# Performance work log

Measured on AMD Instinct MI355X. Metric: run time of the kernel, lower is better.

Reference implementation:

```python
import jax, jax.numpy as jnp
import numpy as np

def setup_inputs() -> dict:
    key = jax.random.key(0)
    k1, k2 = jax.random.split(key)
    B, C = 65536, 1000
    outputs = jax.random.normal(k1, (B, C), dtype=jnp.float32)
    labels = jax.random.randint(k2, (B,), 0, C, dtype=jnp.int64)
    return {"outputs": outputs, "labels": labels}

def reference(outputs, labels):
    B = outputs.shape[0]
    # ground-truth score per row: [B, 1]
    ground = jnp.take_along_axis(outputs, labels[:, None].astype(jnp.int32), axis=1)
    # hinge margin per class: max(0, y_j - y_true + 1); j == label contributes exactly 1
    margins = jnp.maximum(outputs - ground + 1.0, 0.0)
    per_row = jnp.sum(margins, axis=1) - 1.0  # remove the j == label term
    loss = jnp.sum(per_row) / B
    correct_count = jnp.sum(jnp.argmax(outputs, axis=1) == labels)
    return (loss, correct_count)
```

## Files before the change

### kernel.cpp

```cpp
#include <hip/hip_runtime.h>
#include <hip/hip_bf16.h>
#include <math.h>


#define BLOCK 256
#define GRID 1024

__global__ __launch_bounds__(BLOCK) void msrp_kernel(
    const float* __restrict__ outp, const int* __restrict__ labels,
    float* __restrict__ dst, int B, int C) {
  const int lane = threadIdx.x & 63;
  const int wave_in_block = threadIdx.x >> 6;
  const int wave_id = (blockIdx.x * blockDim.x + threadIdx.x) >> 6;
  const int n_waves = (gridDim.x * blockDim.x) >> 6;
  const int C4 = C >> 2;

  float loss_acc = 0.0f;
  int correct_acc = 0;

  for (int row = wave_id; row < B; row += n_waves) {
    const float* rowp = outp + (size_t)row * (size_t)C;
    const int label = labels[row];
    const float ground = rowp[label];
    const float base = 1.0f - ground;

    const float4* rp4 = (const float4*)rowp;
    float s = 0.0f;
    float mx = -INFINITY;
    int mi = 0x7fffffff;

    for (int j = lane; j < C4; j += 64) {
      float4 v = rp4[j];
      s += fmaxf(v.x + base, 0.0f) + fmaxf(v.y + base, 0.0f) +
           fmaxf(v.z + base, 0.0f) + fmaxf(v.w + base, 0.0f);
      const int j4 = j << 2;
      if (v.x > mx) { mx = v.x; mi = j4; }
      if (v.y > mx) { mx = v.y; mi = j4 + 1; }
      if (v.z > mx) { mx = v.z; mi = j4 + 2; }
      if (v.w > mx) { mx = v.w; mi = j4 + 3; }
    }
    for (int j = (C4 << 2) + lane; j < C; j += 64) {
      float v = rowp[j];
      s += fmaxf(v + base, 0.0f);
      if (v > mx) { mx = v; mi = j; }
    }

    for (int off = 32; off > 0; off >>= 1) {
      s += __shfl_down(s, off, 64);
      float omx = __shfl_down(mx, off, 64);
      int omi = __shfl_down(mi, off, 64);
      if (omx > mx || (omx == mx && omi < mi)) { mx = omx; mi = omi; }
    }

    if (lane == 0) {
      loss_acc += s - 1.0f;
      correct_acc += (mi == label) ? 1 : 0;
    }
  }

  __shared__ float ls[BLOCK / 64];
  __shared__ int cs[BLOCK / 64];
  if (lane == 0) { ls[wave_in_block] = loss_acc; cs[wave_in_block] = correct_acc; }
  __syncthreads();
  if (threadIdx.x == 0) {
    float L = 0.0f;
    int cc = 0;
    for (int w = 0; w < BLOCK / 64; ++w) { L += ls[w]; cc += cs[w]; }
    atomicAdd(&dst[0], L / (float)B);
    atomicAdd(&dst[1], (float)cc);
  }
}

extern "C" void kernel_launch(void* const* d_in, const int* in_sizes, int n_in,
                              void* d_out, int out_size, void* d_ws, size_t ws_size,
                              hipStream_t stream) {
  const float* outp = (const float*)d_in[0];
  const int* labels = (const int*)d_in[1];
  float* dst = (float*)d_out;

  const int B = in_sizes[1];
  const int C = in_sizes[0] / B;

  hipMemsetAsync(d_out, 0, (size_t)out_size * sizeof(float), stream);

  msrp_kernel<<<GRID, BLOCK, 0, stream>>>(outp, labels, dst, B, C);
}
```

Measured before the change: 370.4 us.

## Replace argmax with ground-violation ballot and defer reductions to a finalize kernel

Instead of a per-row argmax with index tracking and a shuffle reduction, each lane only flags elements that beat the ground-truth score, with ties broken by a lower index. A single ballot per row then decides whether the row is correct. The hinge sum is kept per lane across all rows and reduced once per wave. Each wave now handles a contiguous chunk of rows whose labels and ground values are preloaded with one lane per row. The memset and atomics are replaced by per-block partials plus a one-block finalize kernel. Rows per wave is computed as B/NWAVE, so any remainder rows are silently dropped when B is not a multiple of NWAVE, and it also assumes at most 64 rows per wave.

```diff
diff --git a/kernel.cpp b/kernel.cpp
--- a/kernel.cpp
+++ b/kernel.cpp
@@ -1,87 +1,114 @@
 #include <hip/hip_runtime.h>
-#include <hip/hip_bf16.h>
 #include <math.h>
 
 
 #define BLOCK 256
-#define GRID 1024
+#define GRID1 2048
+#define WPB   (BLOCK / 64)
+#define NWAVE (GRID1 * WPB)
 
-__global__ __launch_bounds__(BLOCK) void msrp_kernel(
+__global__ __launch_bounds__(BLOCK) void msrp_partial(
     const float* __restrict__ outp, const int* __restrict__ labels,
-    float* __restrict__ dst, int B, int C) {
-  const int lane = threadIdx.x & 63;
-  const int wave_in_block = threadIdx.x >> 6;
-  const int wave_id = (blockIdx.x * blockDim.x + threadIdx.x) >> 6;
-  const int n_waves = (gridDim.x * blockDim.x) >> 6;
+    float* __restrict__ partS, int* __restrict__ partC, int B, int C) {
+  const int lane    = threadIdx.x & 63;
+  const int wib     = threadIdx.x >> 6;
+  const int wave_id = blockIdx.x * WPB + wib;
+  const int R       = B / NWAVE;
+  const int r0      = wave_id * R;
+
+  int   mylab = 0;
+  float myg   = 0.0f;
+  if (lane < R && r0 + lane < B) {
+    mylab = labels[r0 + lane];
+    myg   = outp[(size_t)(r0 + lane) * C + mylab];
+  }
+
+  float s = 0.0f;
+  int correct = 0;
   const int C4 = C >> 2;
 
-  float loss_acc = 0.0f;
-  int correct_acc = 0;
+  for (int k = 0; k < R; ++k) {
+    const int row = r0 + k;
+    if (row >= B) break;
+    const int   label = __shfl(mylab, k, 64);
+    const float g     = __shfl(myg, k, 64);
+    const float base  = 1.0f - g;
+    const float4* rp4 = (const float4*)(outp + (size_t)row * C);
 
-  for (int row = wave_id; row < B; row += n_waves) {
-    const float* rowp = outp + (size_t)row * (size_t)C;
-    const int label = labels[row];
-    const float ground = rowp[label];
-    const float base = 1.0f - ground;
-
-    const float4* rp4 = (const float4*)rowp;
-    float s = 0.0f;
-    float mx = -INFINITY;
-    int mi = 0x7fffffff;
-
+    bool viol = false;
     for (int j = lane; j < C4; j += 64) {
       float4 v = rp4[j];
       s += fmaxf(v.x + base, 0.0f) + fmaxf(v.y + base, 0.0f) +
            fmaxf(v.z + base, 0.0f) + fmaxf(v.w + base, 0.0f);
       const int j4 = j << 2;
-      if (v.x > mx) { mx = v.x; mi = j4; }
-      if (v.y > mx) { mx = v.y; mi = j4 + 1; }
-      if (v.z > mx) { mx = v.z; mi = j4 + 2; }
-      if (v.w > mx) { mx = v.w; mi = j4 + 3; }
+      viol |= (v.x > g) | ((v.x == g) & (j4     < label));
+      viol |= (v.y > g) | ((v.y == g) & (j4 + 1 < label));
+      viol |= (v.z > g) | ((v.z == g) & (j4 + 2 < label));
+      viol |= (v.w > g) | ((v.w == g) & (j4 + 3 < label));
     }
+    const float* rowp = (const float*)rp4;
     for (int j = (C4 << 2) + lane; j < C; j += 64) {
       float v = rowp[j];
       s += fmaxf(v + base, 0.0f);
-      if (v > mx) { mx = v; mi = j; }
+      viol |= (v > g) | ((v == g) & (j < label));
     }
 
-    for (int off = 32; off > 0; off >>= 1) {
-      s += __shfl_down(s, off, 64);
-      float omx = __shfl_down(mx, off, 64);
-      int omi = __shfl_down(mi, off, 64);
-      if (omx > mx || (omx == mx && omi < mi)) { mx = omx; mi = omi; }
-    }
-
-    if (lane == 0) {
-      loss_acc += s - 1.0f;
-      correct_acc += (mi == label) ? 1 : 0;
-    }
+    unsigned long long m = __ballot(viol);
+    if (lane == 0) correct += (m == 0ULL) ? 1 : 0;
   }
 
-  __shared__ float ls[BLOCK / 64];
-  __shared__ int cs[BLOCK / 64];
-  if (lane == 0) { ls[wave_in_block] = loss_acc; cs[wave_in_block] = correct_acc; }
+  for (int off = 32; off > 0; off >>= 1) s += __shfl_down(s, off, 64);
+
+  __shared__ float ls[WPB];
+  __shared__ int   cs[WPB];
+  if (lane == 0) { ls[wib] = s; cs[wib] = correct; }
   __syncthreads();
   if (threadIdx.x == 0) {
-    float L = 0.0f;
-    int cc = 0;
-    for (int w = 0; w < BLOCK / 64; ++w) { L += ls[w]; cc += cs[w]; }
-    atomicAdd(&dst[0], L / (float)B);
-    atomicAdd(&dst[1], (float)cc);
+    float S = 0.0f; int cc = 0;
+    for (int w = 0; w < WPB; ++w) { S += ls[w]; cc += cs[w]; }
+    partS[blockIdx.x] = S;
+    partC[blockIdx.x] = cc;
+  }
+}
+
+__global__ __launch_bounds__(BLOCK) void msrp_finalize(
+    const float* __restrict__ partS, const int* __restrict__ partC,
+    float* __restrict__ dst, int B, int nPart) {
+  const int tid = threadIdx.x;
+  float s = 0.0f; int c = 0;
+  for (int i = tid; i < nPart; i += BLOCK) { s += partS[i]; c += partC[i]; }
+
+  const int lane = tid & 63;
+  const int wib  = tid >> 6;
+  for (int off = 32; off > 0; off >>= 1) {
+    s += __shfl_down(s, off, 64);
+    c += __shfl_down(c, off, 64);
+  }
+  __shared__ float ls[WPB];
+  __shared__ int   cs[WPB];
+  if (lane == 0) { ls[wib] = s; cs[wib] = c; }
+  __syncthreads();
+  if (tid == 0) {
+    float S = 0.0f; int cc = 0;
+    for (int w = 0; w < WPB; ++w) { S += ls[w]; cc += cs[w]; }
+    dst[0] = S / (float)B - 1.0f;
+    dst[1] = (float)cc;
   }
 }
 
 extern "C" void kernel_launch(void* const* d_in, const int* in_sizes, int n_in,
                               void* d_out, int out_size, void* d_ws, size_t ws_size,
                               hipStream_t stream) {
-  const float* outp = (const float*)d_in[0];
-  const int* labels = (const int*)d_in[1];
-  float* dst = (float*)d_out;
+  const float* outp   = (const float*)d_in[0];
+  const int*   labels = (const int*)d_in[1];
+  float*       dst    = (float*)d_out;
 
   const int B = in_sizes[1];
   const int C = in_sizes[0] / B;
 
-  hipMemsetAsync(d_out, 0, (size_t)out_size * sizeof(float), stream);
+  float* partS = (float*)d_ws;
+  int*   partC = (int*)(partS + GRID1);
 
-  msrp_kernel<<<GRID, BLOCK, 0, stream>>>(outp, labels, dst, B, C);
+  msrp_partial<<<GRID1, BLOCK, 0, stream>>>(outp, labels, partS, partC, B, C);
+  msrp_finalize<<<1, BLOCK, 0, stream>>>(partS, partC, dst, B, GRID1);
 }
```

New measurement: 358.9 us. 1.03x faster.
